# Optimization experiments

Measured on AMD Instinct MI355X. Metric: run time of the kernel, lower is better.

Reference implementation:

```python
import jax, jax.numpy as jnp
import numpy as np

K = 3
STRIDE = 1
PAD = K // 2
GN_GROUPS = 32
EPS = 1e-5


def _conv(x, w, b, stride, pad):
    y = jax.lax.conv_general_dilated(
        x, w, window_strides=(stride, stride),
        padding=[(pad, pad), (pad, pad)],
        dimension_numbers=("NCHW", "OIHW", "NCHW"))
    return y + b[None, :, None, None]


def _bilinear_gather(img, ys, xs):
    # img: [B,C,H,W]; ys/xs: [B,P,Ho,Wo] float sampling coords (zero padding outside)
    B, C, H, W = img.shape
    y0 = jnp.floor(ys)
    x0 = jnp.floor(xs)
    y1, x1 = y0 + 1.0, x0 + 1.0
    wy1 = ys - y0  # weight toward y1
    wx1 = xs - x0
    wy0 = 1.0 - wy1
    wx0 = 1.0 - wx1
    img_flat = img.reshape(B, C, H * W)

    def corner(yc, xc, wgt):
        yi = yc.astype(jnp.int32)
        xi = xc.astype(jnp.int32)
        valid = (yi >= 0) & (yi < H) & (xi >= 0) & (xi < W)
        idx = jnp.clip(yi, 0, H - 1) * W + jnp.clip(xi, 0, W - 1)  # [B,P,Ho,Wo]
        Bp, P, Ho, Wo = idx.shape
        idx_f = jnp.broadcast_to(idx.reshape(B, 1, P * Ho * Wo), (B, C, P * Ho * Wo))
        vals = jnp.take_along_axis(img_flat, idx_f, axis=2).reshape(B, C, P, Ho, Wo)
        w_eff = jnp.where(valid, wgt, 0.0)[:, None]  # [B,1,P,Ho,Wo]
        return vals * w_eff

    out = (corner(y0, x0, wy0 * wx0) + corner(y0, x1, wy0 * wx1)
           + corner(y1, x0, wy1 * wx0) + corner(y1, x1, wy1 * wx1))
    return out  # [B,C,P,Ho,Wo]


def _deform_conv_gn_relu(x, w_off, b_off, w, b, gamma, beta):
    B, C_in, H, W = x.shape
    C_out = w.shape[0]
    P = K * K
    # offset-predicting conv: [B, 2*P, Ho, Wo], channel order (dy0,dx0,dy1,dx1,...)
    off = _conv(x, w_off, b_off, STRIDE, PAD)
    Ho, Wo = off.shape[2], off.shape[3]
    off = off.reshape(B, P, 2, Ho, Wo)
    dy, dx = off[:, :, 0], off[:, :, 1]  # [B,P,Ho,Wo]
    ky, kx = jnp.meshgrid(jnp.arange(K, dtype=x.dtype), jnp.arange(K, dtype=x.dtype), indexing="ij")
    ky, kx = ky.reshape(P), kx.reshape(P)
    base_y = (jnp.arange(Ho, dtype=x.dtype) * STRIDE - PAD)
    base_x = (jnp.arange(Wo, dtype=x.dtype) * STRIDE - PAD)
    ys = base_y[None, None, :, None] + ky[None, :, None, None] + dy
    xs = base_x[None, None, None, :] + kx[None, :, None, None] + dx
    cols = _bilinear_gather(x, ys, xs)  # [B,C_in,P,Ho,Wo]
    y = jnp.einsum("bcphw,ocp->bohw", cols, w.reshape(C_out, C_in, P)) + b[None, :, None, None]
    # GroupNorm(32, C_out)
    G = GN_GROUPS
    yg = y.reshape(B, G, (C_out // G) * Ho * Wo)
    mu = yg.mean(axis=2, keepdims=True)
    var = yg.var(axis=2, keepdims=True)
    yn = ((yg - mu) * jax.lax.rsqrt(var + EPS)).reshape(B, C_out, Ho, Wo)
    yn = yn * gamma[None, :, None, None] + beta[None, :, None, None]
    return jax.nn.relu(yn)


def setup_inputs() -> dict:
    key = jax.random.key(0)
    ks = jax.random.split(key, 7)
    B, C_in, C_out, H, W = 4, 256, 256, 64, 64
    P = K * K
    fan = C_in * P
    x = jax.random.normal(ks[0], (B, C_in, H, W), dtype=jnp.float32)
    w_off = jax.random.normal(ks[1], (2 * P, C_in, K, K), dtype=jnp.float32) * 0.01
    b_off = jnp.zeros((2 * P,), dtype=jnp.float32)
    w = jax.random.normal(ks[2], (C_out, C_in, K, K), dtype=jnp.float32) / np.sqrt(fan)
    b = jax.random.normal(ks[3], (C_out,), dtype=jnp.float32) * 0.01
    gamma = jnp.ones((C_out,), dtype=jnp.float32)
    beta = jnp.zeros((C_out,), dtype=jnp.float32)
    return {"x": x, "w_off": w_off, "b_off": b_off, "w": w, "b": b, "gamma": gamma, "beta": beta}


def reference(x, w_off, b_off, w, b, gamma, beta):
    return _deform_conv_gn_relu(x, w_off, b_off, w, b, gamma, beta)
```

## Files before the change

kernel.cpp:

```cpp
#include <hip/hip_runtime.h>
#include <hip/hip_bf16.h>

using bf16 = __hip_bfloat16;
typedef __attribute__((ext_vector_type(4))) float f32x4;
typedef __attribute__((ext_vector_type(2))) float f32x2;
typedef __attribute__((ext_vector_type(8))) __bf16 bf16x8;
typedef __attribute__((ext_vector_type(4))) __bf16 bf16x4;

#define CIN 256
#define COUT 256
#define HW 4096
#define NB 4
#define NTOT 16384
#define KDIM 2304

__global__ __launch_bounds__(256) void k_pre(const float* __restrict__ x,
                                             const float* __restrict__ w,
                                             const float* __restrict__ wof,
                                             bf16* __restrict__ xt,
                                             bf16* __restrict__ A,
                                             float* __restrict__ wt,
                                             float* __restrict__ gstats) {
  int bid = blockIdx.x;
  int tid = threadIdx.x;
  if (bid < 2048) {
    __shared__ float t[64][33];
    int ct = bid & 3;
    int hwt = (bid >> 2) & 127;
    int b = bid >> 9;
    int c0 = ct * 64, hw0 = hwt * 32;
    const float* xb = x + (size_t)b * CIN * HW;
    int cc = tid >> 5, ww = tid & 31;
#pragma unroll
    for (int pass = 0; pass < 8; ++pass)
      t[cc + pass * 8][ww] = xb[(size_t)(c0 + cc + pass * 8) * HW + hw0 + ww];
    __syncthreads();
    int hwl = tid >> 3, ce = (tid & 7) * 8;
    bf16x8 v;
#pragma unroll
    for (int e = 0; e < 8; ++e) v[e] = (__bf16)t[ce + e][hwl];
    *(bf16x8*)(xt + ((size_t)b * HW + hw0 + hwl) * CIN + c0 + ce) = v;
  } else if (bid < 4352) {
    int i = (bid - 2048) * 256 + tid;
    int o = i / KDIM, r = i % KDIM;
    int p = r >> 8, c = r & 255;
    A[i] = __float2bfloat16(w[((size_t)o * 256 + c) * 9 + p]);
  } else if (bid < 4514) {
    int i = (bid - 4352) * 256 + tid;
    if (i < 18 * CIN * 9) {
      int oc = i % 18;
      int cp = i / 18;
      int c = cp / 9, p = cp % 9;
      wt[i] = wof[((size_t)oc * CIN + c) * 9 + p];
    }
  } else {
    gstats[tid] = 0.f;
  }
}

__global__ __launch_bounds__(256) void k_convoff2(const float* __restrict__ x,
                                                  const float* __restrict__ wt,
                                                  float* __restrict__ part) {
  __shared__ float lds[8][6][68];
  int bid = blockIdx.x;
  int chunk = bid & 7;
  int rt = (bid >> 3) & 15;
  int b = bid >> 7;
  int tid = threadIdx.x;
  int wq = tid & 63, r = tid >> 6;
  int h0 = rt * 4;
  int c0 = chunk * 32;

  if (tid < 96) {
    int cl = tid / 12, rem = tid % 12;
    lds[cl][rem >> 1][(rem & 1) ? 66 : 1] = 0.f;
  }

  float acc[18];
#pragma unroll
  for (int o = 0; o < 18; ++o) acc[o] = 0.f;

  int ch = tid >> 5, l32 = tid & 31;
  const float* xb = x + (size_t)b * CIN * HW;

  for (int cs = 0; cs < 32; cs += 8) {
    __syncthreads();
    const float* xp = xb + (size_t)(c0 + cs + ch) * HW;
#pragma unroll
    for (int r6 = 0; r6 < 6; ++r6) {
      int hh = h0 - 1 + r6;
      f32x2 v = {0.f, 0.f};
      if ((unsigned)hh < 64u) v = *(const f32x2*)(xp + hh * 64 + l32 * 2);
      *(f32x2*)&lds[ch][r6][2 + l32 * 2] = v;
    }
    __syncthreads();
#pragma unroll
    for (int cl = 0; cl < 8; ++cl) {
      int c = c0 + cs + cl;
      const float* wc = wt + (size_t)c * 9 * 18;
      float xv[9];
#pragma unroll
      for (int ky = 0; ky < 3; ++ky)
#pragma unroll
        for (int kx = 0; kx < 3; ++kx)
          xv[ky * 3 + kx] = lds[cl][r + ky][1 + wq + kx];
#pragma unroll
      for (int p = 0; p < 9; ++p)
#pragma unroll
        for (int o = 0; o < 18; ++o)
          acc[o] = fmaf(xv[p], wc[p * 18 + o], acc[o]);
    }
  }

  float* pp = part + (size_t)chunk * (NB * 18 * HW) + (size_t)b * 18 * HW +
              (h0 + r) * 64 + wq;
#pragma unroll
  for (int o = 0; o < 18; ++o) pp[(size_t)o * HW] = acc[o];
}

__global__ __launch_bounds__(256) void k_offreduce(const float* __restrict__ part,
                                                   const float* __restrict__ boff,
                                                   float* __restrict__ off) {
  int i = blockIdx.x * 256 + threadIdx.x;
  int e0 = i * 4;
  int oc = (e0 >> 12) % 18;
  float bo = boff[oc];
  f32x4 s = {bo, bo, bo, bo};
#pragma unroll
  for (int c = 0; c < 8; ++c) s += *(const f32x4*)(part + (size_t)c * (NB * 18 * HW) + e0);
  *(f32x4*)(off + e0) = s;
}

__global__ __launch_bounds__(256) void k_gather(const bf16* __restrict__ xt,
                                                const float* __restrict__ off,
                                                bf16* __restrict__ colsT) {
  int tid = threadIdx.x;
  int wv = tid >> 6, l = tid & 63;
  int n = blockIdx.x * 4 + wv;
  int hw = n & 4095;
  int b = n >> 12;
  int h = hw >> 6, wq = hw & 63;
  const bf16* xtb = xt + (size_t)b * HW * CIN + l * 4;
  const float* offb = off + (size_t)b * 18 * HW + hw;
  bf16* outp = colsT + (size_t)n * KDIM + l * 4;
#pragma unroll
  for (int p = 0; p < 9; ++p) {
    float dy = offb[(size_t)(2 * p) * HW];
    float dx = offb[(size_t)(2 * p + 1) * HW];
    float ysf = (float)(h - 1 + p / 3) + dy;
    float xsf = (float)(wq - 1 + p % 3) + dx;
    float y0f = floorf(ysf), x0f = floorf(xsf);
    float wy1 = ysf - y0f, wx1 = xsf - x0f;
    float wy0 = 1.f - wy1, wx0 = 1.f - wx1;
    int y0 = (int)y0f, x0 = (int)x0f;
    int y1 = y0 + 1, x1 = x0 + 1;
    float w00 = wy0 * wx0, w01 = wy0 * wx1, w10 = wy1 * wx0, w11 = wy1 * wx1;
    bool vy0 = (unsigned)y0 < 64u, vy1 = (unsigned)y1 < 64u;
    bool vx0 = (unsigned)x0 < 64u, vx1 = (unsigned)x1 < 64u;
    w00 = (vy0 && vx0) ? w00 : 0.f;
    w01 = (vy0 && vx1) ? w01 : 0.f;
    w10 = (vy1 && vx0) ? w10 : 0.f;
    w11 = (vy1 && vx1) ? w11 : 0.f;
    int y0c = min(max(y0, 0), 63), y1c = min(max(y1, 0), 63);
    int x0c = min(max(x0, 0), 63), x1c = min(max(x1, 0), 63);
    bf16x4 c00 = *(const bf16x4*)(xtb + (size_t)(y0c * 64 + x0c) * CIN);
    bf16x4 c01 = *(const bf16x4*)(xtb + (size_t)(y0c * 64 + x1c) * CIN);
    bf16x4 c10 = *(const bf16x4*)(xtb + (size_t)(y1c * 64 + x0c) * CIN);
    bf16x4 c11 = *(const bf16x4*)(xtb + (size_t)(y1c * 64 + x1c) * CIN);
    bf16x4 o;
#pragma unroll
    for (int k = 0; k < 4; ++k) {
      float v = w00 * (float)c00[k] + w01 * (float)c01[k] +
                w10 * (float)c10[k] + w11 * (float)c11[k];
      o[k] = (__bf16)v;
    }
    *(bf16x4*)(outp + p * 256) = o;
  }
}

__global__ __launch_bounds__(256) void k_gemm(const bf16* __restrict__ A,
                                              const bf16* __restrict__ Bt,
                                              const float* __restrict__ bias,
                                              float* __restrict__ Y,
                                              float* __restrict__ gsum,
                                              float* __restrict__ gsq) {
  __shared__ bf16 As[3][256 * 64];
  __shared__ bf16 Bs[3][64 * 64];
  int bid = blockIdx.x;
  int swz = (bid & 7) * 32 + (bid >> 3);
  int n0 = swz * 64;
  int tid = threadIdx.x;
  int lane = tid & 63;
  int wave = tid >> 6;
  int wr = wave * 64;
  f32x4 acc[4][4];
#pragma unroll
  for (int i = 0; i < 4; ++i)
#pragma unroll
    for (int j = 0; j < 4; ++j) acc[i][j] = (f32x4){0.f, 0.f, 0.f, 0.f};

  int srow = tid >> 3;
  int skdst = (tid & 7) * 8;
  int sksrc = ((tid & 7) ^ ((tid >> 3) & 7)) * 8;
  auto stage = [&](int buf, int kt) {
    int k0 = kt * 64;
#pragma unroll
    for (int ps = 0; ps < 8; ++ps) {
      int r = srow + ps * 32;
      __builtin_amdgcn_global_load_lds(
          (const __attribute__((address_space(1))) void*)(A + (size_t)r * KDIM + k0 + sksrc),
          (__attribute__((address_space(3))) void*)(&As[buf][r * 64 + skdst]), 16, 0, 0);
    }
#pragma unroll
    for (int ps = 0; ps < 2; ++ps) {
      int r = srow + ps * 32;
      __builtin_amdgcn_global_load_lds(
          (const __attribute__((address_space(1))) void*)(Bt + (size_t)(n0 + r) * KDIM + k0 + sksrc),
          (__attribute__((address_space(3))) void*)(&Bs[buf][r * 64 + skdst]), 16, 0, 0);
    }
  };

  int rl = lane & 15;
  int kb = (lane >> 4) * 8;
  int xorv = (rl & 7) * 8;

  constexpr int NT = KDIM / 64;
  stage(0, 0);
  stage(1, 1);

  auto kstep = [&](int kt, int cur, int stg, bool dostage, bool last) {
    if (last) asm volatile("s_waitcnt vmcnt(0)" ::: "memory");
    else      asm volatile("s_waitcnt vmcnt(10)" ::: "memory");
    __builtin_amdgcn_s_barrier();
    if (dostage) stage(stg, kt + 2);
    const bf16* as = As[cur];
    const bf16* bs = Bs[cur];
#pragma unroll
    for (int kh = 0; kh < 2; ++kh) {
      int kc = (kh * 32 + kb) ^ xorv;
      bf16x8 af[4], bfr[4];
#pragma unroll
      for (int i = 0; i < 4; ++i)
        af[i] = *(const bf16x8*)(as + (wr + i * 16 + rl) * 64 + kc);
#pragma unroll
      for (int j = 0; j < 4; ++j)
        bfr[j] = *(const bf16x8*)(bs + (j * 16 + rl) * 64 + kc);
#pragma unroll
      for (int i = 0; i < 4; ++i)
#pragma unroll
        for (int j = 0; j < 4; ++j)
          acc[i][j] = __builtin_amdgcn_mfma_f32_16x16x32_bf16(af[i], bfr[j], acc[i][j], 0, 0, 0);
    }
  };

  for (int kt = 0; kt < NT - 3; kt += 3) {
    kstep(kt + 0, 0, 2, true, false);
    kstep(kt + 1, 1, 0, true, false);
    kstep(kt + 2, 2, 1, true, false);
  }
  kstep(NT - 3, 0, 2, true, false);
  kstep(NT - 2, 1, 0, false, false);
  kstep(NT - 1, 2, 0, false, true);

  int cl = lane & 15, rg = (lane >> 4) * 4;
  int b = n0 >> 12;
#pragma unroll
  for (int i = 0; i < 4; ++i) {
    int obase = wr + i * 16;
    int ob = obase + rg;
    float s = 0.f, s2 = 0.f;
#pragma unroll
    for (int j = 0; j < 4; ++j) {
      int nn = n0 + j * 16 + cl;
#pragma unroll
      for (int r = 0; r < 4; ++r) {
        float yv = acc[i][j][r] + bias[ob + r];
        Y[(size_t)(ob + r) * NTOT + nn] = yv;
        s += yv;
        s2 = fmaf(yv, yv, s2);
      }
    }
#pragma unroll
    for (int mk = 1; mk <= 16; mk <<= 1) {
      s += __shfl_xor(s, mk);
      s2 += __shfl_xor(s2, mk);
    }
    if ((lane & 31) == 0) {
      int g = (obase >> 3) + (lane >> 5);
      atomicAdd(&gsum[b * 32 + g], s);
      atomicAdd(&gsq[b * 32 + g], s2);
    }
  }
}

__global__ __launch_bounds__(256) void k_apply(const float* __restrict__ Y,
                                               const float* __restrict__ gsum,
                                               const float* __restrict__ gsq,
                                               const float* __restrict__ gamma,
                                               const float* __restrict__ beta,
                                               float* __restrict__ out) {
  int i = blockIdx.x * 256 + threadIdx.x;
  int hw4 = i & 1023;
  int o = (i >> 10) & 255;
  int b = i >> 18;
  int g = o >> 3;
  float mu = gsum[b * 32 + g] * (1.f / 32768.f);
  float var = gsq[b * 32 + g] * (1.f / 32768.f) - mu * mu;
  float rs = rsqrtf(var + 1e-5f);
  float s = rs * gamma[o];
  float t = beta[o] - mu * s;
  f32x4 v = *(const f32x4*)(Y + (size_t)o * NTOT + b * HW + hw4 * 4);
  f32x4 r;
#pragma unroll
  for (int k = 0; k < 4; ++k) r[k] = fmaxf(v[k] * s + t, 0.f);
  *(f32x4*)(out + (size_t)i * 4) = r;
}

extern "C" void kernel_launch(void* const* d_in, const int* in_sizes, int n_in,
                              void* d_out, int out_size, void* d_ws, size_t ws_size,
                              hipStream_t stream) {
  const float* x = (const float*)d_in[0];
  const float* w_off = (const float*)d_in[1];
  const float* b_off = (const float*)d_in[2];
  const float* w = (const float*)d_in[3];
  const float* bias = (const float*)d_in[4];
  const float* gamma = (const float*)d_in[5];
  const float* beta = (const float*)d_in[6];
  float* out = (float*)d_out;
  char* ws = (char*)d_ws;

  bf16* xt = (bf16*)(ws);
  float* offb = (float*)(ws + 8388608);
  bf16* Abf = (bf16*)(ws + 8388608 + 1179648);
  bf16* colsT = (bf16*)(ws + 8388608 + 2 * 1179648);
  float* Y = (float*)(ws + 8388608 + 2 * 1179648 + 75497472);
  float* gsum = (float*)(ws + 8388608 + 16777216 + 2 * 1179648 + 75497472);
  float* gsq = gsum + 128;

  float* wt = (float*)colsT;
  float* part = (float*)((char*)colsT + 262144);

  k_pre<<<4515, 256, 0, stream>>>(x, w, w_off, xt, Abf, wt, gsum);
  k_convoff2<<<512, 256, 0, stream>>>(x, wt, part);
  k_offreduce<<<288, 256, 0, stream>>>(part, b_off, offb);
  k_gather<<<4096, 256, 0, stream>>>(xt, offb, colsT);
  k_gemm<<<256, 256, 0, stream>>>(Abf, colsT, bias, Y, gsum, gsq);
  k_apply<<<4096, 256, 0, stream>>>(Y, gsum, gsq, gamma, beta, out);
}
```

Baseline: 128.3 us.

## Split GEMM K dimension in two, store bf16 partials, add separate GN stats kernel

```diff
diff --git a/kernel.cpp b/kernel.cpp
--- a/kernel.cpp
+++ b/kernel.cpp
@@ -19,8 +19,7 @@
                                              const float* __restrict__ wof,
                                              bf16* __restrict__ xt,
                                              bf16* __restrict__ A,
-                                             float* __restrict__ wt,
-                                             float* __restrict__ gstats) {
+                                             float* __restrict__ wt) {
   int bid = blockIdx.x;
   int tid = threadIdx.x;
   if (bid < 2048) {
@@ -45,7 +44,7 @@
     int o = i / KDIM, r = i % KDIM;
     int p = r >> 8, c = r & 255;
     A[i] = __float2bfloat16(w[((size_t)o * 256 + c) * 9 + p]);
-  } else if (bid < 4514) {
+  } else {
     int i = (bid - 4352) * 256 + tid;
     if (i < 18 * CIN * 9) {
       int oc = i % 18;
@@ -53,8 +52,6 @@
       int c = cp / 9, p = cp % 9;
       wt[i] = wof[((size_t)oc * CIN + c) * 9 + p];
     }
-  } else {
-    gstats[tid] = 0.f;
   }
 }
 
@@ -181,14 +178,14 @@
 __global__ __launch_bounds__(256) void k_gemm(const bf16* __restrict__ A,
                                               const bf16* __restrict__ Bt,
                                               const float* __restrict__ bias,
-                                              float* __restrict__ Y,
-                                              float* __restrict__ gsum,
-                                              float* __restrict__ gsq) {
-  __shared__ bf16 As[3][256 * 64];
-  __shared__ bf16 Bs[3][64 * 64];
+                                              bf16* __restrict__ Y0,
+                                              bf16* __restrict__ Y1) {
+  __shared__ bf16 As[2][256 * 64];
+  __shared__ bf16 Bs[2][64 * 64];
   int bid = blockIdx.x;
-  int swz = (bid & 7) * 32 + (bid >> 3);
-  int n0 = swz * 64;
+  int swz = (bid & 7) * 64 + (bid >> 3);
+  int n0 = (swz >> 1) * 64;
+  int khalf = swz & 1;
   int tid = threadIdx.x;
   int lane = tid & 63;
   int wave = tid >> 6;
@@ -202,8 +199,9 @@
   int srow = tid >> 3;
   int skdst = (tid & 7) * 8;
   int sksrc = ((tid & 7) ^ ((tid >> 3) & 7)) * 8;
+  int kbase = khalf * 18;
   auto stage = [&](int buf, int kt) {
-    int k0 = kt * 64;
+    int k0 = (kbase + kt) * 64;
 #pragma unroll
     for (int ps = 0; ps < 8; ++ps) {
       int r = srow + ps * 32;
@@ -220,21 +218,15 @@
     }
   };
 
+  stage(0, 0);
   int rl = lane & 15;
   int kb = (lane >> 4) * 8;
   int xorv = (rl & 7) * 8;
-
-  constexpr int NT = KDIM / 64;
-  stage(0, 0);
-  stage(1, 1);
-
-  auto kstep = [&](int kt, int cur, int stg, bool dostage, bool last) {
-    if (last) asm volatile("s_waitcnt vmcnt(0)" ::: "memory");
-    else      asm volatile("s_waitcnt vmcnt(10)" ::: "memory");
-    __builtin_amdgcn_s_barrier();
-    if (dostage) stage(stg, kt + 2);
-    const bf16* as = As[cur];
-    const bf16* bs = Bs[cur];
+  for (int kt = 0; kt < 18; ++kt) {
+    __syncthreads();
+    if (kt + 1 < 18) stage((kt + 1) & 1, kt + 1);
+    const bf16* as = As[kt & 1];
+    const bf16* bs = Bs[kt & 1];
 #pragma unroll
     for (int kh = 0; kh < 2; ++kh) {
       int kc = (kh * 32 + kb) ^ xorv;
@@ -251,69 +243,92 @@
         for (int j = 0; j < 4; ++j)
           acc[i][j] = __builtin_amdgcn_mfma_f32_16x16x32_bf16(af[i], bfr[j], acc[i][j], 0, 0, 0);
     }
-  };
-
-  for (int kt = 0; kt < NT - 3; kt += 3) {
-    kstep(kt + 0, 0, 2, true, false);
-    kstep(kt + 1, 1, 0, true, false);
-    kstep(kt + 2, 2, 1, true, false);
-  }
-  kstep(NT - 3, 0, 2, true, false);
-  kstep(NT - 2, 1, 0, false, false);
-  kstep(NT - 1, 2, 0, false, true);
+  }
 
   int cl = lane & 15, rg = (lane >> 4) * 4;
-  int b = n0 >> 12;
+  bf16* Yp = khalf ? Y1 : Y0;
 #pragma unroll
   for (int i = 0; i < 4; ++i) {
-    int obase = wr + i * 16;
-    int ob = obase + rg;
-    float s = 0.f, s2 = 0.f;
+    int ob = wr + i * 16 + rg;
 #pragma unroll
     for (int j = 0; j < 4; ++j) {
       int nn = n0 + j * 16 + cl;
 #pragma unroll
       for (int r = 0; r < 4; ++r) {
-        float yv = acc[i][j][r] + bias[ob + r];
-        Y[(size_t)(ob + r) * NTOT + nn] = yv;
-        s += yv;
-        s2 = fmaf(yv, yv, s2);
+        float yv = acc[i][j][r] + (khalf ? 0.f : bias[ob + r]);
+        Yp[(size_t)(ob + r) * NTOT + nn] = __float2bfloat16(yv);
       }
     }
-#pragma unroll
-    for (int mk = 1; mk <= 16; mk <<= 1) {
-      s += __shfl_xor(s, mk);
-      s2 += __shfl_xor(s2, mk);
-    }
-    if ((lane & 31) == 0) {
-      int g = (obase >> 3) + (lane >> 5);
-      atomicAdd(&gsum[b * 32 + g], s);
-      atomicAdd(&gsq[b * 32 + g], s2);
-    }
-  }
-}
-
-__global__ __launch_bounds__(256) void k_apply(const float* __restrict__ Y,
-                                               const float* __restrict__ gsum,
-                                               const float* __restrict__ gsq,
+  }
+}
+
+__global__ __launch_bounds__(256) void k_gnstats(const bf16* __restrict__ Y0,
+                                                 const bf16* __restrict__ Y1,
+                                                 float* __restrict__ mu_,
+                                                 float* __restrict__ rs_) {
+  int b = blockIdx.x >> 5, g = blockIdx.x & 31;
+  int tid = threadIdx.x;
+  float s = 0.f, s2 = 0.f;
+  for (int i = tid; i < 4096; i += 256) {
+    int ol = i >> 9, pos = i & 511;
+    size_t off = (size_t)(g * 8 + ol) * NTOT + b * HW + pos * 8;
+    bf16x8 v0 = *(const bf16x8*)(Y0 + off);
+    bf16x8 v1 = *(const bf16x8*)(Y1 + off);
+#pragma unroll
+    for (int k = 0; k < 8; ++k) {
+      float y = (float)v0[k] + (float)v1[k];
+      s += y;
+      s2 = fmaf(y, y, s2);
+    }
+  }
+#pragma unroll
+  for (int o = 32; o > 0; o >>= 1) {
+    s += __shfl_down(s, o);
+    s2 += __shfl_down(s2, o);
+  }
+  __shared__ float red[8];
+  int wv = tid >> 6;
+  if ((tid & 63) == 0) { red[wv] = s; red[wv + 4] = s2; }
+  __syncthreads();
+  if (tid == 0) {
+    float S = red[0] + red[1] + red[2] + red[3];
+    float S2 = red[4] + red[5] + red[6] + red[7];
+    float mu = S * (1.f / 32768.f);
+    float var = S2 * (1.f / 32768.f) - mu * mu;
+    mu_[b * 32 + g] = mu;
+    rs_[b * 32 + g] = rsqrtf(var + 1e-5f);
+  }
+}
+
+__global__ __launch_bounds__(256) void k_apply(const bf16* __restrict__ Y0,
+                                               const bf16* __restrict__ Y1,
+                                               const float* __restrict__ mu_,
+                                               const float* __restrict__ rs_,
                                                const float* __restrict__ gamma,
                                                const float* __restrict__ beta,
                                                float* __restrict__ out) {
   int i = blockIdx.x * 256 + threadIdx.x;
-  int hw4 = i & 1023;
-  int o = (i >> 10) & 255;
-  int b = i >> 18;
+  int hw8 = i & 511;
+  int o = (i >> 9) & 255;
+  int b = i >> 17;
   int g = o >> 3;
-  float mu = gsum[b * 32 + g] * (1.f / 32768.f);
-  float var = gsq[b * 32 + g] * (1.f / 32768.f) - mu * mu;
-  float rs = rsqrtf(var + 1e-5f);
+  float mu = mu_[b * 32 + g];
+  float rs = rs_[b * 32 + g];
   float s = rs * gamma[o];
   float t = beta[o] - mu * s;
-  f32x4 v = *(const f32x4*)(Y + (size_t)o * NTOT + b * HW + hw4 * 4);
-  f32x4 r;
-#pragma unroll
-  for (int k = 0; k < 4; ++k) r[k] = fmaxf(v[k] * s + t, 0.f);
-  *(f32x4*)(out + (size_t)i * 4) = r;
+  size_t off = (size_t)o * NTOT + b * HW + hw8 * 8;
+  bf16x8 v0 = *(const bf16x8*)(Y0 + off);
+  bf16x8 v1 = *(const bf16x8*)(Y1 + off);
+  float* op = out + ((size_t)b * COUT + o) * HW + hw8 * 8;
+  f32x4 r0, r1;
+#pragma unroll
+  for (int k = 0; k < 4; ++k)
+    r0[k] = fmaxf(((float)v0[k] + (float)v1[k]) * s + t, 0.f);
+#pragma unroll
+  for (int k = 0; k < 4; ++k)
+    r1[k] = fmaxf(((float)v0[k + 4] + (float)v1[k + 4]) * s + t, 0.f);
+  *(f32x4*)op = r0;
+  *(f32x4*)(op + 4) = r1;
 }
 
 extern "C" void kernel_launch(void* const* d_in, const int* in_sizes, int n_in,
@@ -333,17 +348,19 @@
   float* offb = (float*)(ws + 8388608);
   bf16* Abf = (bf16*)(ws + 8388608 + 1179648);
   bf16* colsT = (bf16*)(ws + 8388608 + 2 * 1179648);
-  float* Y = (float*)(ws + 8388608 + 2 * 1179648 + 75497472);
-  float* gsum = (float*)(ws + 8388608 + 16777216 + 2 * 1179648 + 75497472);
-  float* gsq = gsum + 128;
+  bf16* Y0 = (bf16*)(ws + 8388608 + 2 * 1179648 + 75497472);
+  bf16* Y1 = Y0 + (size_t)COUT * NTOT;
+  float* mus = (float*)(ws + 2 * 8388608 + 2 * 1179648 + 75497472 + 8388608);
+  float* rss = mus + 128;
 
   float* wt = (float*)colsT;
   float* part = (float*)((char*)colsT + 262144);
 
-  k_pre<<<4515, 256, 0, stream>>>(x, w, w_off, xt, Abf, wt, gsum);
+  k_pre<<<4514, 256, 0, stream>>>(x, w, w_off, xt, Abf, wt);
   k_convoff2<<<512, 256, 0, stream>>>(x, wt, part);
   k_offreduce<<<288, 256, 0, stream>>>(part, b_off, offb);
   k_gather<<<4096, 256, 0, stream>>>(xt, offb, colsT);
-  k_gemm<<<256, 256, 0, stream>>>(Abf, colsT, bias, Y, gsum, gsq);
-  k_apply<<<4096, 256, 0, stream>>>(Y, gsum, gsq, gamma, beta, out);
-}
+  k_gemm<<<512, 256, 0, stream>>>(Abf, colsT, bias, Y0, Y1);
+  k_gnstats<<<128, 256, 0, stream>>>(Y0, Y1, mus, rss);
+  k_apply<<<2048, 256, 0, stream>>>(Y0, Y1, mus, rss, gamma, beta, out);
+}
```

Result: slower. 132.2 us (+3.0%).
